# Optimization experiments

Measured on AMD Instinct MI355X. Metric: run time of the kernel, lower is better.

## Reference

```python
import jax, jax.numpy as jnp
import numpy as np

N_NODES = 40000
N_EDGES = 640000
D = 128
BN_EPS = 1e-5


def setup_inputs() -> dict:
    key = jax.random.key(0)
    k1, k2, k3, k4 = jax.random.split(key, 4)
    x = jax.random.normal(k1, (N_NODES, D), dtype=jnp.float32)
    edge_index = jax.random.randint(k2, (2, N_EDGES), 0, N_NODES, dtype=jnp.int64)
    W = jax.random.normal(k3, (D, D), dtype=jnp.float32) * (1.0 / np.sqrt(D))
    b = jax.random.normal(k4, (D,), dtype=jnp.float32) * 0.01
    gamma = jnp.ones((D,), dtype=jnp.float32)
    beta = jnp.zeros((D,), dtype=jnp.float32)
    return {"x": x, "edge_index": edge_index, "W": W, "b": b,
            "gamma": gamma, "beta": beta}


def reference(x, edge_index, W, b, gamma, beta):
    num_nodes = x.shape[0]
    # linear projection: [N, D_in] @ [D_in, D_out]
    h = x @ W.T + b
    src, dst = edge_index[0], edge_index[1]
    # gather messages from source nodes, scatter-add into destinations
    msgs = jax.ops.segment_sum(h[src], dst, num_segments=num_nodes)  # [N, D]
    # in-degree of each destination node, clamped to >= 1
    deg = jax.ops.segment_sum(jnp.ones_like(dst, dtype=h.dtype), dst,
                              num_segments=num_nodes)
    deg = jnp.maximum(deg, 1.0)
    h = h + msgs / deg[:, None]
    # BatchNorm1d (training mode: biased batch statistics over nodes)
    mean = jnp.mean(h, axis=0)
    var = jnp.mean(jnp.square(h - mean), axis=0)
    out = (h - mean) * jax.lax.rsqrt(var + BN_EPS) * gamma + beta
    return jax.nn.relu(out)
```

## Files before the change

### kernel.cpp

```cpp
#include <hip/hip_runtime.h>

#define NN 40000
#define NE 640000
#define DD 128
#define MAXDEG 64
#define BN_EPS 1e-5f

typedef __attribute__((ext_vector_type(8))) short short8;
typedef __attribute__((ext_vector_type(4))) float f32x4;

__device__ __forceinline__ unsigned int rb16(float x) {
  unsigned int u = __float_as_uint(x);
  return (u + 0x7fffu + ((u >> 16) & 1u)) >> 16;
}

#define PADK 136
__global__ __launch_bounds__(256) void gemm_kernel(
    const float* __restrict__ x, const float* __restrict__ W,
    const float* __restrict__ bias, unsigned int* __restrict__ hbf) {
  __shared__ unsigned short xs[128 * PADK];
  __shared__ unsigned short ws[128 * PADK];
  const int tid = threadIdx.x;
  const int node0 = blockIdx.x * 128;

#pragma unroll
  for (int it = 0; it < 16; ++it) {
    const int flat = it * 256 + tid;
    const int row = flat >> 5;
    const int c4 = flat & 31;
    const int gn = node0 + row;
    float4 v = make_float4(0.f, 0.f, 0.f, 0.f);
    if (gn < NN) v = *reinterpret_cast<const float4*>(x + (size_t)gn * DD + c4 * 4);
    ushort4 p;
    p.x = (unsigned short)rb16(v.x);
    p.y = (unsigned short)rb16(v.y);
    p.z = (unsigned short)rb16(v.z);
    p.w = (unsigned short)rb16(v.w);
    *reinterpret_cast<ushort4*>(&xs[row * PADK + c4 * 4]) = p;
    const float4 wv = *reinterpret_cast<const float4*>(W + (size_t)row * DD + c4 * 4);
    ushort4 q;
    q.x = (unsigned short)rb16(wv.x);
    q.y = (unsigned short)rb16(wv.y);
    q.z = (unsigned short)rb16(wv.z);
    q.w = (unsigned short)rb16(wv.w);
    *reinterpret_cast<ushort4*>(&ws[row * PADK + c4 * 4]) = q;
  }
  __syncthreads();

  const int wave = tid >> 6;
  const int lane = tid & 63;
  const int m = lane & 15;
  const int g = lane >> 4;
  f32x4 acc[2][8];
#pragma unroll
  for (int t = 0; t < 2; ++t)
#pragma unroll
    for (int ct = 0; ct < 8; ++ct) acc[t][ct] = (f32x4){0.f, 0.f, 0.f, 0.f};

#pragma unroll
  for (int ks = 0; ks < 4; ++ks) {
    const int ko = ks * 32 + g * 8;
    short8 a[2], b[8];
#pragma unroll
    for (int t = 0; t < 2; ++t)
      a[t] = *reinterpret_cast<const short8*>(&xs[(wave * 32 + t * 16 + m) * PADK + ko]);
#pragma unroll
    for (int ct = 0; ct < 8; ++ct)
      b[ct] = *reinterpret_cast<const short8*>(&ws[(ct * 16 + m) * PADK + ko]);
#pragma unroll
    for (int t = 0; t < 2; ++t)
#pragma unroll
      for (int ct = 0; ct < 8; ++ct)
        acc[t][ct] = __builtin_amdgcn_mfma_f32_16x16x32_bf16(a[t], b[ct], acc[t][ct], 0, 0, 0);
  }
  __syncthreads();

#pragma unroll
  for (int t = 0; t < 2; ++t) {
#pragma unroll
    for (int ct = 0; ct < 8; ++ct) {
      const int ch = ct * 16 + m;
      const float bv = bias[ch];
#pragma unroll
      for (int reg = 0; reg < 4; ++reg) {
        const int nrow = wave * 32 + t * 16 + g * 4 + reg;
        xs[nrow * PADK + ch] = (unsigned short)rb16(acc[t][ct][reg] + bv);
      }
    }
  }
  __syncthreads();
#pragma unroll
  for (int it = 0; it < 8; ++it) {
    const int flat = it * 256 + tid;
    const int row = flat >> 4;
    const int c8 = flat & 15;
    const int gn = node0 + row;
    if (gn < NN) {
      const uint4 o = *reinterpret_cast<const uint4*>(&xs[row * PADK + c8 * 8]);
      *reinterpret_cast<uint4*>(hbf + (size_t)gn * 64 + c8 * 4) = o;
    }
  }
}

__global__ __launch_bounds__(256) void bucket_kernel(
    const int* __restrict__ ei, int* __restrict__ cursors,
    unsigned short* __restrict__ esorted) {
  const int e = blockIdx.x * 256 + threadIdx.x;
  if (e < NE) {
    const int s = ei[e];
    const int d = ei[NE + e];
    const int p = atomicAdd(&cursors[d], 1);
    if (p < MAXDEG) esorted[(size_t)d * MAXDEG + p] = (unsigned short)s;
  }
}

__global__ __launch_bounds__(256) void gather_kernel(
    const unsigned int* __restrict__ hbf,
    const unsigned short* __restrict__ esorted, const int* __restrict__ cursors,
    float* __restrict__ v_out, float* __restrict__ sums) {
  const int tid = threadIdx.x;
  const int wv = tid >> 6;
  const int lane = tid & 63;
  const int q = lane >> 4;
  const int c = lane & 15;
  const int nWaves = gridDim.x * 4;
  float s8[8], q8[8];
#pragma unroll
  for (int j = 0; j < 8; ++j) { s8[j] = 0.f; q8[j] = 0.f; }

  for (int n = blockIdx.x * 4 + wv; n < NN; n += nWaves) {
    const int deg = cursors[n];
    const int dcl = min(deg, MAXDEG);
    const int base = n * MAXDEG;
    float acc[8];
#pragma unroll
    for (int j = 0; j < 8; ++j) acc[j] = 0.f;

    for (int i0 = 0; i0 < dcl; i0 += 16) {
      int id[4];
      float w[4];
#pragma unroll
      for (int j = 0; j < 4; ++j) {
        const int e = i0 + q + 4 * j;
        const int raw = (int)esorted[base + min(e, MAXDEG - 1)];
        const bool vld = e < dcl;
        id[j] = vld ? raw : n;
        w[j] = vld ? 1.f : 0.f;
      }
#pragma unroll
      for (int j = 0; j < 4; ++j) {
        const uint4 u = *reinterpret_cast<const uint4*>(hbf + (size_t)id[j] * 64 + c * 4);
        acc[0] = fmaf(__uint_as_float(u.x << 16), w[j], acc[0]);
        acc[1] = fmaf(__uint_as_float(u.x & 0xffff0000u), w[j], acc[1]);
        acc[2] = fmaf(__uint_as_float(u.y << 16), w[j], acc[2]);
        acc[3] = fmaf(__uint_as_float(u.y & 0xffff0000u), w[j], acc[3]);
        acc[4] = fmaf(__uint_as_float(u.z << 16), w[j], acc[4]);
        acc[5] = fmaf(__uint_as_float(u.z & 0xffff0000u), w[j], acc[5]);
        acc[6] = fmaf(__uint_as_float(u.w << 16), w[j], acc[6]);
        acc[7] = fmaf(__uint_as_float(u.w & 0xffff0000u), w[j], acc[7]);
      }
    }
#pragma unroll
    for (int j = 0; j < 8; ++j) {
      acc[j] += __shfl_xor(acc[j], 16, 64);
      acc[j] += __shfl_xor(acc[j], 32, 64);
    }
    if (q == 0) {
      const float rdeg = 1.0f / (float)max(deg, 1);
      const uint4 su = *reinterpret_cast<const uint4*>(hbf + (size_t)n * 64 + c * 4);
      float v[8];
      v[0] = __uint_as_float(su.x << 16) + acc[0] * rdeg;
      v[1] = __uint_as_float(su.x & 0xffff0000u) + acc[1] * rdeg;
      v[2] = __uint_as_float(su.y << 16) + acc[2] * rdeg;
      v[3] = __uint_as_float(su.y & 0xffff0000u) + acc[3] * rdeg;
      v[4] = __uint_as_float(su.z << 16) + acc[4] * rdeg;
      v[5] = __uint_as_float(su.z & 0xffff0000u) + acc[5] * rdeg;
      v[6] = __uint_as_float(su.w << 16) + acc[6] * rdeg;
      v[7] = __uint_as_float(su.w & 0xffff0000u) + acc[7] * rdeg;
      *reinterpret_cast<float4*>(v_out + (size_t)n * DD + c * 8) =
          make_float4(v[0], v[1], v[2], v[3]);
      *reinterpret_cast<float4*>(v_out + (size_t)n * DD + c * 8 + 4) =
          make_float4(v[4], v[5], v[6], v[7]);
#pragma unroll
      for (int j = 0; j < 8; ++j) {
        s8[j] += v[j];
        q8[j] += v[j] * v[j];
      }
    }
  }
  __shared__ float redS[4][128];
  __shared__ float redQ[4][128];
  if (q == 0) {
#pragma unroll
    for (int j = 0; j < 8; ++j) {
      redS[wv][c * 8 + j] = s8[j];
      redQ[wv][c * 8 + j] = q8[j];
    }
  }
  __syncthreads();
  if (tid < 128) {
    const float S = redS[0][tid] + redS[1][tid] + redS[2][tid] + redS[3][tid];
    const float Q = redQ[0][tid] + redQ[1][tid] + redQ[2][tid] + redQ[3][tid];
    const int r = blockIdx.x & 7;
    unsafeAtomicAdd(&sums[r * 256 + tid], S);
    unsafeAtomicAdd(&sums[r * 256 + 128 + tid], Q);
  }
}

__global__ __launch_bounds__(256) void normalize_kernel(
    const float* __restrict__ sums, const float* __restrict__ gamma,
    const float* __restrict__ beta, float* __restrict__ out) {
  __shared__ float sc[128];
  __shared__ float sh[128];
  const int tid = threadIdx.x;
  if (tid < 128) {
    float S = 0.f, Q = 0.f;
#pragma unroll
    for (int r = 0; r < 8; ++r) {
      S += sums[r * 256 + tid];
      Q += sums[r * 256 + 128 + tid];
    }
    const float inv_n = 1.0f / (float)NN;
    const float mean = S * inv_n;
    const float var = Q * inv_n - mean * mean;
    const float inv = rsqrtf(var + BN_EPS);
    const float g = gamma[tid] * inv;
    sc[tid] = g;
    sh[tid] = beta[tid] - mean * g;
  }
  __syncthreads();
  const long total4 = (long)NN * DD / 4;
  for (long i = blockIdx.x * 256L + tid; i < total4; i += (long)gridDim.x * 256L) {
    const int c4 = (int)(i & 31);
    const float4 v = *reinterpret_cast<const float4*>(out + i * 4);
    const float4 scv = *reinterpret_cast<const float4*>(&sc[c4 * 4]);
    const float4 shv = *reinterpret_cast<const float4*>(&sh[c4 * 4]);
    float4 o;
    o.x = fmaxf(v.x * scv.x + shv.x, 0.f);
    o.y = fmaxf(v.y * scv.y + shv.y, 0.f);
    o.z = fmaxf(v.z * scv.z + shv.z, 0.f);
    o.w = fmaxf(v.w * scv.w + shv.w, 0.f);
    *reinterpret_cast<float4*>(out + i * 4) = o;
  }
}

extern "C" void kernel_launch(void* const* d_in, const int* in_sizes, int n_in,
                              void* d_out, int out_size, void* d_ws, size_t ws_size,
                              hipStream_t stream) {
  const float* x     = (const float*)d_in[0];
  const int*   ei    = (const int*)d_in[1];
  const float* W     = (const float*)d_in[2];
  const float* b     = (const float*)d_in[3];
  const float* gamma = (const float*)d_in[4];
  const float* beta  = (const float*)d_in[5];
  float* out = (float*)d_out;

  unsigned int*   hbf     = (unsigned int*)d_ws;
  unsigned short* esorted = (unsigned short*)(hbf + (size_t)NN * 64);
  int*            cursors = (int*)(esorted + (size_t)NN * MAXDEG);
  float*          sums    = (float*)(cursors + NN);

  hipMemsetAsync(cursors, 0, (size_t)(NN + 8 * 256) * sizeof(int), stream);

  gemm_kernel<<<(NN + 127) / 128, 256, 0, stream>>>(x, W, b, hbf);
  bucket_kernel<<<(NE + 255) / 256, 256, 0, stream>>>(ei, cursors, esorted);
  gather_kernel<<<2560, 256, 0, stream>>>(hbf, esorted, cursors, out, sums);
  normalize_kernel<<<1280, 256, 0, stream>>>(sums, gamma, beta, out);
}
```

Before: 156.6 us.

## Fuse bucketing, gather and batchnorm into one cooperative grid-synced kernel

Replaces the memset, bucket, gather and normalize launches with a single cooperative kernel that zeroes the counters, buckets edges, gathers neighbours, reduces statistics and normalizes, separated by grid.sync barriers. Each wave loads its node's neighbour list once into registers and broadcasts indices by shuffle, and prefetches the next node's degree and list while working on the current one. This removes launch gaps and repeated per-iteration esorted loads. In exchange, the grid is limited to occupancy-sized persistent blocks (capped at 1024), and grid-wide barriers add cost. A fallback runs the old multi-kernel path if the cooperative launch fails.

```diff
diff --git a/kernel.cpp b/kernel.cpp
--- a/kernel.cpp
+++ b/kernel.cpp
@@ -1,10 +1,14 @@
 #include <hip/hip_runtime.h>
+#include <hip/hip_cooperative_groups.h>
+
+namespace cg = cooperative_groups;
 
 #define NN 40000
 #define NE 640000
 #define DD 128
 #define MAXDEG 64
 #define BN_EPS 1e-5f
+#define MAXBLK 1024
 
 typedef __attribute__((ext_vector_type(8))) short short8;
 typedef __attribute__((ext_vector_type(4))) float f32x4;
@@ -102,6 +106,168 @@
   }
 }
 
+__device__ __forceinline__ void gather_node(
+    const unsigned int* __restrict__ hbf, int n, int deg, int sraw,
+    int q, int c, float* __restrict__ vout8, bool* wrote) {
+  const int dcl = min(deg, MAXDEG);
+  float acc[8];
+#pragma unroll
+  for (int j = 0; j < 8; ++j) acc[j] = 0.f;
+  for (int i0 = 0; i0 < dcl; i0 += 16) {
+    int id[4];
+    float w[4];
+#pragma unroll
+    for (int j = 0; j < 4; ++j) {
+      const int e = i0 + q + 4 * j;
+      const int idv = __shfl(sraw, min(e, MAXDEG - 1), 64);
+      const bool vld = e < dcl;
+      id[j] = vld ? idv : n;
+      w[j] = vld ? 1.f : 0.f;
+    }
+#pragma unroll
+    for (int j = 0; j < 4; ++j) {
+      const uint4 u = *reinterpret_cast<const uint4*>(hbf + (size_t)id[j] * 64 + c * 4);
+      acc[0] = fmaf(__uint_as_float(u.x << 16), w[j], acc[0]);
+      acc[1] = fmaf(__uint_as_float(u.x & 0xffff0000u), w[j], acc[1]);
+      acc[2] = fmaf(__uint_as_float(u.y << 16), w[j], acc[2]);
+      acc[3] = fmaf(__uint_as_float(u.y & 0xffff0000u), w[j], acc[3]);
+      acc[4] = fmaf(__uint_as_float(u.z << 16), w[j], acc[4]);
+      acc[5] = fmaf(__uint_as_float(u.z & 0xffff0000u), w[j], acc[5]);
+      acc[6] = fmaf(__uint_as_float(u.w << 16), w[j], acc[6]);
+      acc[7] = fmaf(__uint_as_float(u.w & 0xffff0000u), w[j], acc[7]);
+    }
+  }
+#pragma unroll
+  for (int j = 0; j < 8; ++j) {
+    acc[j] += __shfl_xor(acc[j], 16, 64);
+    acc[j] += __shfl_xor(acc[j], 32, 64);
+  }
+  *wrote = (q == 0);
+  if (q == 0) {
+    const float rdeg = 1.0f / (float)max(deg, 1);
+    const uint4 su = *reinterpret_cast<const uint4*>(hbf + (size_t)n * 64 + c * 4);
+    vout8[0] = __uint_as_float(su.x << 16) + acc[0] * rdeg;
+    vout8[1] = __uint_as_float(su.x & 0xffff0000u) + acc[1] * rdeg;
+    vout8[2] = __uint_as_float(su.y << 16) + acc[2] * rdeg;
+    vout8[3] = __uint_as_float(su.y & 0xffff0000u) + acc[3] * rdeg;
+    vout8[4] = __uint_as_float(su.z << 16) + acc[4] * rdeg;
+    vout8[5] = __uint_as_float(su.z & 0xffff0000u) + acc[5] * rdeg;
+    vout8[6] = __uint_as_float(su.w << 16) + acc[6] * rdeg;
+    vout8[7] = __uint_as_float(su.w & 0xffff0000u) + acc[7] * rdeg;
+  }
+}
+
+__global__ __launch_bounds__(256, 4) void fused_kernel(
+    const int* __restrict__ ei, const unsigned int* __restrict__ hbf,
+    unsigned short* __restrict__ esorted, int* __restrict__ cursors,
+    float* __restrict__ sums, const float* __restrict__ gamma,
+    const float* __restrict__ beta, float* __restrict__ out) {
+  cg::grid_group grid = cg::this_grid();
+  const int tid = threadIdx.x;
+  const int bid = blockIdx.x;
+  const int gsz = gridDim.x * 256;
+  const int gt = bid * 256 + tid;
+
+  for (int i = gt; i < NN + 8 * 256; i += gsz) cursors[i] = 0;
+  grid.sync();
+
+  for (int e = gt; e < NE; e += gsz) {
+    const int s = ei[e];
+    const int d = ei[NE + e];
+    const int p = atomicAdd(&cursors[d], 1);
+    if (p < MAXDEG) esorted[d * MAXDEG + p] = (unsigned short)s;
+  }
+  grid.sync();
+
+  const int wv = tid >> 6;
+  const int lane = tid & 63;
+  const int q = lane >> 4;
+  const int c = lane & 15;
+  const int nW = gridDim.x * 4;
+  const int wid = bid * 4 + wv;
+  float s8[8], q8[8];
+#pragma unroll
+  for (int j = 0; j < 8; ++j) { s8[j] = 0.f; q8[j] = 0.f; }
+
+  int n = wid;
+  int deg = 0, sraw = 0;
+  if (n < NN) {
+    deg = cursors[n];
+    sraw = (int)esorted[n * MAXDEG + lane];
+  }
+  while (n < NN) {
+    const int n2 = n + nW;
+    int deg2 = 0, sraw2 = 0;
+    if (n2 < NN) {
+      deg2 = cursors[n2];
+      sraw2 = (int)esorted[n2 * MAXDEG + lane];
+    }
+    float v[8];
+    bool wrote;
+    gather_node(hbf, n, deg, sraw, q, c, v, &wrote);
+    if (wrote) {
+      *reinterpret_cast<float4*>(out + (size_t)n * DD + c * 8) =
+          make_float4(v[0], v[1], v[2], v[3]);
+      *reinterpret_cast<float4*>(out + (size_t)n * DD + c * 8 + 4) =
+          make_float4(v[4], v[5], v[6], v[7]);
+#pragma unroll
+      for (int j = 0; j < 8; ++j) {
+        s8[j] += v[j];
+        q8[j] += v[j] * v[j];
+      }
+    }
+    n = n2;
+    deg = deg2;
+    sraw = sraw2;
+  }
+  __shared__ float redS[4][128];
+  __shared__ float redQ[4][128];
+  if (q == 0) {
+#pragma unroll
+    for (int j = 0; j < 8; ++j) {
+      redS[wv][c * 8 + j] = s8[j];
+      redQ[wv][c * 8 + j] = q8[j];
+    }
+  }
+  __syncthreads();
+  if (tid < 128) {
+    const float S = redS[0][tid] + redS[1][tid] + redS[2][tid] + redS[3][tid];
+    const float Q = redQ[0][tid] + redQ[1][tid] + redQ[2][tid] + redQ[3][tid];
+    const int r = bid & 7;
+    unsafeAtomicAdd(&sums[r * 256 + tid], S);
+    unsafeAtomicAdd(&sums[r * 256 + 128 + tid], Q);
+  }
+  grid.sync();
+
+  __shared__ float sc[128];
+  __shared__ float sh[128];
+  if (tid < 128) {
+    float S = 0.f, Q = 0.f;
+#pragma unroll
+    for (int r = 0; r < 8; ++r) {
+      S += sums[r * 256 + tid];
+      Q += sums[r * 256 + 128 + tid];
+    }
+    const float inv_n = 1.0f / (float)NN;
+    const float mean = S * inv_n;
+    const float var = Q * inv_n - mean * mean;
+    const float inv = rsqrtf(var + BN_EPS);
+    const float g = gamma[tid] * inv;
+    sc[tid] = g;
+    sh[tid] = beta[tid] - mean * g;
+  }
+  __syncthreads();
+  const int ch = lane * 2;
+  const float2 scv = make_float2(sc[ch], sc[ch + 1]);
+  const float2 shv = make_float2(sh[ch], sh[ch + 1]);
+  for (int nn = wid; nn < NN; nn += nW) {
+    float2 v = *reinterpret_cast<const float2*>(out + (size_t)nn * DD + ch);
+    v.x = fmaxf(v.x * scv.x + shv.x, 0.f);
+    v.y = fmaxf(v.y * scv.y + shv.y, 0.f);
+    *reinterpret_cast<float2*>(out + (size_t)nn * DD + ch) = v;
+  }
+}
+
 __global__ __launch_bounds__(256) void bucket_kernel(
     const int* __restrict__ ei, int* __restrict__ cursors,
     unsigned short* __restrict__ esorted) {
@@ -110,7 +276,7 @@
     const int s = ei[e];
     const int d = ei[NE + e];
     const int p = atomicAdd(&cursors[d], 1);
-    if (p < MAXDEG) esorted[(size_t)d * MAXDEG + p] = (unsigned short)s;
+    if (p < MAXDEG) esorted[d * MAXDEG + p] = (unsigned short)s;
   }
 }
 
@@ -123,60 +289,18 @@
   const int lane = tid & 63;
   const int q = lane >> 4;
   const int c = lane & 15;
-  const int nWaves = gridDim.x * 4;
+  const int nW = gridDim.x * 4;
+  const int wid = blockIdx.x * 4 + wv;
   float s8[8], q8[8];
 #pragma unroll
   for (int j = 0; j < 8; ++j) { s8[j] = 0.f; q8[j] = 0.f; }
-
-  for (int n = blockIdx.x * 4 + wv; n < NN; n += nWaves) {
+  for (int n = wid; n < NN; n += nW) {
     const int deg = cursors[n];
-    const int dcl = min(deg, MAXDEG);
-    const int base = n * MAXDEG;
-    float acc[8];
-#pragma unroll
-    for (int j = 0; j < 8; ++j) acc[j] = 0.f;
-
-    for (int i0 = 0; i0 < dcl; i0 += 16) {
-      int id[4];
-      float w[4];
-#pragma unroll
-      for (int j = 0; j < 4; ++j) {
-        const int e = i0 + q + 4 * j;
-        const int raw = (int)esorted[base + min(e, MAXDEG - 1)];
-        const bool vld = e < dcl;
-        id[j] = vld ? raw : n;
-        w[j] = vld ? 1.f : 0.f;
-      }
-#pragma unroll
-      for (int j = 0; j < 4; ++j) {
-        const uint4 u = *reinterpret_cast<const uint4*>(hbf + (size_t)id[j] * 64 + c * 4);
-        acc[0] = fmaf(__uint_as_float(u.x << 16), w[j], acc[0]);
-        acc[1] = fmaf(__uint_as_float(u.x & 0xffff0000u), w[j], acc[1]);
-        acc[2] = fmaf(__uint_as_float(u.y << 16), w[j], acc[2]);
-        acc[3] = fmaf(__uint_as_float(u.y & 0xffff0000u), w[j], acc[3]);
-        acc[4] = fmaf(__uint_as_float(u.z << 16), w[j], acc[4]);
-        acc[5] = fmaf(__uint_as_float(u.z & 0xffff0000u), w[j], acc[5]);
-        acc[6] = fmaf(__uint_as_float(u.w << 16), w[j], acc[6]);
-        acc[7] = fmaf(__uint_as_float(u.w & 0xffff0000u), w[j], acc[7]);
-      }
-    }
-#pragma unroll
-    for (int j = 0; j < 8; ++j) {
-      acc[j] += __shfl_xor(acc[j], 16, 64);
-      acc[j] += __shfl_xor(acc[j], 32, 64);
-    }
-    if (q == 0) {
-      const float rdeg = 1.0f / (float)max(deg, 1);
-      const uint4 su = *reinterpret_cast<const uint4*>(hbf + (size_t)n * 64 + c * 4);
-      float v[8];
-      v[0] = __uint_as_float(su.x << 16) + acc[0] * rdeg;
-      v[1] = __uint_as_float(su.x & 0xffff0000u) + acc[1] * rdeg;
-      v[2] = __uint_as_float(su.y << 16) + acc[2] * rdeg;
-      v[3] = __uint_as_float(su.y & 0xffff0000u) + acc[3] * rdeg;
-      v[4] = __uint_as_float(su.z << 16) + acc[4] * rdeg;
-      v[5] = __uint_as_float(su.z & 0xffff0000u) + acc[5] * rdeg;
-      v[6] = __uint_as_float(su.w << 16) + acc[6] * rdeg;
-      v[7] = __uint_as_float(su.w & 0xffff0000u) + acc[7] * rdeg;
+    const int sraw = (int)esorted[n * MAXDEG + lane];
+    float v[8];
+    bool wrote;
+    gather_node(hbf, n, deg, sraw, q, c, v, &wrote);
+    if (wrote) {
       *reinterpret_cast<float4*>(v_out + (size_t)n * DD + c * 8) =
           make_float4(v[0], v[1], v[2], v[3]);
       *reinterpret_cast<float4*>(v_out + (size_t)n * DD + c * 8 + 4) =
@@ -260,10 +384,25 @@
   int*            cursors = (int*)(esorted + (size_t)NN * MAXDEG);
   float*          sums    = (float*)(cursors + NN);
 
-  hipMemsetAsync(cursors, 0, (size_t)(NN + 8 * 256) * sizeof(int), stream);
-
   gemm_kernel<<<(NN + 127) / 128, 256, 0, stream>>>(x, W, b, hbf);
-  bucket_kernel<<<(NE + 255) / 256, 256, 0, stream>>>(ei, cursors, esorted);
-  gather_kernel<<<2560, 256, 0, stream>>>(hbf, esorted, cursors, out, sums);
-  normalize_kernel<<<1280, 256, 0, stream>>>(sums, gamma, beta, out);
-}
+
+  int occ = 0;
+  hipError_t qerr =
+      hipOccupancyMaxActiveBlocksPerMultiprocessor(&occ, fused_kernel, 256, 0);
+  int nblk = (qerr == hipSuccess && occ > 0) ? occ * 256 : 0;
+  if (nblk > MAXBLK) nblk = MAXBLK;
+
+  hipError_t lerr = hipErrorUnknown;
+  if (nblk > 0) {
+    void* args[] = {(void*)&ei, (void*)&hbf, (void*)&esorted, (void*)&cursors,
+                    (void*)&sums, (void*)&gamma, (void*)&beta, (void*)&out};
+    lerr = hipLaunchCooperativeKernel(fused_kernel, dim3(nblk), dim3(256), args,
+                                      0, stream);
+  }
+  if (lerr != hipSuccess) {
+    hipMemsetAsync(cursors, 0, (size_t)(NN + 8 * 256) * sizeof(int), stream);
+    bucket_kernel<<<(NE + 255) / 256, 256, 0, stream>>>(ei, cursors, esorted);
+    gather_kernel<<<2560, 256, 0, stream>>>(hbf, esorted, cursors, out, sums);
+    normalize_kernel<<<1280, 256, 0, stream>>>(sums, gamma, beta, out);
+  }
+}
```

Measured after the change: 345.7 us. 121% more time.

## Fuse GEMM and edge bucketing into one launch; prefetch next node in gather

Applied to the files above, without the earlier changes.

The GEMM and the edge-bucketing kernels are merged into one launch, with extra blocks doing grid-strided bucketing so the two independent stages can run at the same time and one launch is saved. The gather kernel now loads each node's whole neighbor list with one coalesced per-lane read and hands indices out by wave shuffle instead of repeated scalar loads. It also software-prefetches the next node's degree, neighbor list and self row. The risks are extra register pressure and the bucketing blocks, which use no shared memory, still reserving the GEMM kernel's large shared allocation.

```diff
diff --git a/kernel.cpp b/kernel.cpp
--- a/kernel.cpp
+++ b/kernel.cpp
@@ -5,6 +5,9 @@
 #define DD 128
 #define MAXDEG 64
 #define BN_EPS 1e-5f
+#define GEMM_BLKS 313
+#define BUCKET_BLKS 320
+#define PADK 136
 
 typedef __attribute__((ext_vector_type(8))) short short8;
 typedef __attribute__((ext_vector_type(4))) float f32x4;
@@ -14,15 +17,27 @@
   return (u + 0x7fffu + ((u >> 16) & 1u)) >> 16;
 }
 
-#define PADK 136
-__global__ __launch_bounds__(256) void gemm_kernel(
+__global__ __launch_bounds__(256) void fat_kernel(
     const float* __restrict__ x, const float* __restrict__ W,
-    const float* __restrict__ bias, unsigned int* __restrict__ hbf) {
+    const float* __restrict__ bias, unsigned int* __restrict__ hbf,
+    const int* __restrict__ ei, int* __restrict__ cursors,
+    unsigned short* __restrict__ esorted) {
   __shared__ unsigned short xs[128 * PADK];
   __shared__ unsigned short ws[128 * PADK];
   const int tid = threadIdx.x;
+
+  if (blockIdx.x >= GEMM_BLKS) {
+    const int b = blockIdx.x - GEMM_BLKS;
+    for (int e = b * 256 + tid; e < NE; e += BUCKET_BLKS * 256) {
+      const int s = ei[e];
+      const int d = ei[NE + e];
+      const int p = atomicAdd(&cursors[d], 1);
+      if (p < MAXDEG) esorted[d * MAXDEG + p] = (unsigned short)s;
+    }
+    return;
+  }
+
   const int node0 = blockIdx.x * 128;
-
 #pragma unroll
   for (int it = 0; it < 16; ++it) {
     const int flat = it * 256 + tid;
@@ -102,18 +117,6 @@
   }
 }
 
-__global__ __launch_bounds__(256) void bucket_kernel(
-    const int* __restrict__ ei, int* __restrict__ cursors,
-    unsigned short* __restrict__ esorted) {
-  const int e = blockIdx.x * 256 + threadIdx.x;
-  if (e < NE) {
-    const int s = ei[e];
-    const int d = ei[NE + e];
-    const int p = atomicAdd(&cursors[d], 1);
-    if (p < MAXDEG) esorted[(size_t)d * MAXDEG + p] = (unsigned short)s;
-  }
-}
-
 __global__ __launch_bounds__(256) void gather_kernel(
     const unsigned int* __restrict__ hbf,
     const unsigned short* __restrict__ esorted, const int* __restrict__ cursors,
@@ -123,28 +126,42 @@
   const int lane = tid & 63;
   const int q = lane >> 4;
   const int c = lane & 15;
-  const int nWaves = gridDim.x * 4;
+  const int nW = gridDim.x * 4;
+  const int wid = blockIdx.x * 4 + wv;
   float s8[8], q8[8];
 #pragma unroll
   for (int j = 0; j < 8; ++j) { s8[j] = 0.f; q8[j] = 0.f; }
 
-  for (int n = blockIdx.x * 4 + wv; n < NN; n += nWaves) {
-    const int deg = cursors[n];
+  int n = wid;
+  int deg = 0, sraw = 0;
+  uint4 su = make_uint4(0u, 0u, 0u, 0u);
+  if (n < NN) {
+    deg = cursors[n];
+    sraw = (int)esorted[n * MAXDEG + lane];
+    su = *reinterpret_cast<const uint4*>(hbf + (size_t)n * 64 + c * 4);
+  }
+  while (n < NN) {
+    const int n2 = n + nW;
+    int deg2 = 0, sraw2 = 0;
+    uint4 su2 = make_uint4(0u, 0u, 0u, 0u);
+    if (n2 < NN) {
+      deg2 = cursors[n2];
+      sraw2 = (int)esorted[n2 * MAXDEG + lane];
+      su2 = *reinterpret_cast<const uint4*>(hbf + (size_t)n2 * 64 + c * 4);
+    }
     const int dcl = min(deg, MAXDEG);
-    const int base = n * MAXDEG;
     float acc[8];
 #pragma unroll
     for (int j = 0; j < 8; ++j) acc[j] = 0.f;
-
     for (int i0 = 0; i0 < dcl; i0 += 16) {
       int id[4];
       float w[4];
 #pragma unroll
       for (int j = 0; j < 4; ++j) {
         const int e = i0 + q + 4 * j;
-        const int raw = (int)esorted[base + min(e, MAXDEG - 1)];
+        const int idv = __shfl(sraw, min(e, MAXDEG - 1), 64);
         const bool vld = e < dcl;
-        id[j] = vld ? raw : n;
+        id[j] = vld ? idv : n;
         w[j] = vld ? 1.f : 0.f;
       }
 #pragma unroll
@@ -167,7 +184,6 @@
     }
     if (q == 0) {
       const float rdeg = 1.0f / (float)max(deg, 1);
-      const uint4 su = *reinterpret_cast<const uint4*>(hbf + (size_t)n * 64 + c * 4);
       float v[8];
       v[0] = __uint_as_float(su.x << 16) + acc[0] * rdeg;
       v[1] = __uint_as_float(su.x & 0xffff0000u) + acc[1] * rdeg;
@@ -187,6 +203,10 @@
         q8[j] += v[j] * v[j];
       }
     }
+    n = n2;
+    deg = deg2;
+    sraw = sraw2;
+    su = su2;
   }
   __shared__ float redS[4][128];
   __shared__ float redQ[4][128];
@@ -261,9 +281,8 @@
   float*          sums    = (float*)(cursors + NN);
 
   hipMemsetAsync(cursors, 0, (size_t)(NN + 8 * 256) * sizeof(int), stream);
-
-  gemm_kernel<<<(NN + 127) / 128, 256, 0, stream>>>(x, W, b, hbf);
-  bucket_kernel<<<(NE + 255) / 256, 256, 0, stream>>>(ei, cursors, esorted);
+  fat_kernel<<<GEMM_BLKS + BUCKET_BLKS, 256, 0, stream>>>(x, W, b, hbf, ei,
+                                                          cursors, esorted);
   gather_kernel<<<2560, 256, 0, stream>>>(hbf, esorted, cursors, out, sums);
   normalize_kernel<<<1280, 256, 0, stream>>>(sums, gamma, beta, out);
 }
```

Result: faster. 145.9 us (-6.8%).

## Fuse edge bucketing into gather via per-block shared-memory scans; pre-convert W

Applied to the files above, without the earlier changes.

Drops the global atomic bucket kernel and the cursor memset. Each of 256 blocks scans the full destination array and bins the edges whose destinations fall in its own node range into shared-memory slots, then gathers for those nodes. W is converted to bf16 once by a small prep kernel, which also zeroes the sums, and the GEMM reads W straight from global memory instead of staging it in LDS. The cost is that every block rereads the whole 2.5 MB edge-destination array, which amounts to about 650 MB of mostly-L2 traffic in total. Only 256 blocks of 1024 threads are used, which may leave parallelism and occupancy short.

```diff
diff --git a/kernel.cpp b/kernel.cpp
--- a/kernel.cpp
+++ b/kernel.cpp
@@ -3,8 +3,11 @@
 #define NN 40000
 #define NE 640000
 #define DD 128
-#define MAXDEG 64
 #define BN_EPS 1e-5f
+#define GEMM_BLKS 313
+#define PADK 132
+#define SG_BLOCKS 256
+#define NPB 157
 
 typedef __attribute__((ext_vector_type(8))) short short8;
 typedef __attribute__((ext_vector_type(4))) float f32x4;
@@ -14,15 +17,21 @@
   return (u + 0x7fffu + ((u >> 16) & 1u)) >> 16;
 }
 
-#define PADK 136
+__global__ __launch_bounds__(256) void prep_kernel(
+    const float* __restrict__ W, unsigned short* __restrict__ wbf,
+    float* __restrict__ sums) {
+  const int gt = blockIdx.x * 256 + threadIdx.x;
+  const int gsz = gridDim.x * 256;
+  for (int i = gt; i < 8 * 256; i += gsz) sums[i] = 0.f;
+  for (int i = gt; i < DD * DD; i += gsz) wbf[i] = (unsigned short)rb16(W[i]);
+}
+
 __global__ __launch_bounds__(256) void gemm_kernel(
-    const float* __restrict__ x, const float* __restrict__ W,
+    const float* __restrict__ x, const unsigned short* __restrict__ wbf,
     const float* __restrict__ bias, unsigned int* __restrict__ hbf) {
   __shared__ unsigned short xs[128 * PADK];
-  __shared__ unsigned short ws[128 * PADK];
   const int tid = threadIdx.x;
   const int node0 = blockIdx.x * 128;
-
 #pragma unroll
   for (int it = 0; it < 16; ++it) {
     const int flat = it * 256 + tid;
@@ -37,13 +46,6 @@
     p.z = (unsigned short)rb16(v.z);
     p.w = (unsigned short)rb16(v.w);
     *reinterpret_cast<ushort4*>(&xs[row * PADK + c4 * 4]) = p;
-    const float4 wv = *reinterpret_cast<const float4*>(W + (size_t)row * DD + c4 * 4);
-    ushort4 q;
-    q.x = (unsigned short)rb16(wv.x);
-    q.y = (unsigned short)rb16(wv.y);
-    q.z = (unsigned short)rb16(wv.z);
-    q.w = (unsigned short)rb16(wv.w);
-    *reinterpret_cast<ushort4*>(&ws[row * PADK + c4 * 4]) = q;
   }
   __syncthreads();
 
@@ -66,7 +68,7 @@
       a[t] = *reinterpret_cast<const short8*>(&xs[(wave * 32 + t * 16 + m) * PADK + ko]);
 #pragma unroll
     for (int ct = 0; ct < 8; ++ct)
-      b[ct] = *reinterpret_cast<const short8*>(&ws[(ct * 16 + m) * PADK + ko]);
+      b[ct] = *reinterpret_cast<const short8*>(wbf + (ct * 16 + m) * DD + ko);
 #pragma unroll
     for (int t = 0; t < 2; ++t)
 #pragma unroll
@@ -102,49 +104,64 @@
   }
 }
 
-__global__ __launch_bounds__(256) void bucket_kernel(
-    const int* __restrict__ ei, int* __restrict__ cursors,
-    unsigned short* __restrict__ esorted) {
-  const int e = blockIdx.x * 256 + threadIdx.x;
-  if (e < NE) {
-    const int s = ei[e];
-    const int d = ei[NE + e];
-    const int p = atomicAdd(&cursors[d], 1);
-    if (p < MAXDEG) esorted[(size_t)d * MAXDEG + p] = (unsigned short)s;
-  }
-}
-
-__global__ __launch_bounds__(256) void gather_kernel(
-    const unsigned int* __restrict__ hbf,
-    const unsigned short* __restrict__ esorted, const int* __restrict__ cursors,
-    float* __restrict__ v_out, float* __restrict__ sums) {
+__global__ __launch_bounds__(1024) void scangather_kernel(
+    const int* __restrict__ ei, const unsigned int* __restrict__ hbf,
+    float* __restrict__ out, float* __restrict__ sums) {
+  __shared__ unsigned short slots[NPB * 64];
+  __shared__ int cnt[NPB];
+  __shared__ float redS[16][128];
+  __shared__ float redQ[16][128];
   const int tid = threadIdx.x;
+  const int lo = blockIdx.x * NPB;
+  const int hi = min(lo + NPB, NN);
+  const int nloc = hi - lo;
+
+  for (int i = tid; i < NPB; i += 1024) cnt[i] = 0;
+  __syncthreads();
+
+  const int4* d4 = reinterpret_cast<const int4*>(ei + NE);
+  const int* srcA = ei;
+  const int nch = NE / 4;
+  for (int idx = tid; idx < nch; idx += 1024) {
+    const int4 dv = d4[idx];
+    const int e = idx * 4;
+#pragma unroll
+    for (int j = 0; j < 4; ++j) {
+      const int d = (j == 0) ? dv.x : (j == 1) ? dv.y : (j == 2) ? dv.z : dv.w;
+      const int dl = d - lo;
+      if (dl >= 0 && dl < nloc) {
+        const int p = atomicAdd(&cnt[dl], 1);
+        if (p < 64) slots[dl * 64 + p] = (unsigned short)srcA[e + j];
+      }
+    }
+  }
+  __syncthreads();
+
   const int wv = tid >> 6;
   const int lane = tid & 63;
   const int q = lane >> 4;
   const int c = lane & 15;
-  const int nWaves = gridDim.x * 4;
   float s8[8], q8[8];
 #pragma unroll
   for (int j = 0; j < 8; ++j) { s8[j] = 0.f; q8[j] = 0.f; }
 
-  for (int n = blockIdx.x * 4 + wv; n < NN; n += nWaves) {
-    const int deg = cursors[n];
-    const int dcl = min(deg, MAXDEG);
-    const int base = n * MAXDEG;
+  for (int nl = wv; nl < nloc; nl += 16) {
+    const int n = lo + nl;
+    const int deg = cnt[nl];
+    const int dcl = min(deg, 64);
+    const uint4 su = *reinterpret_cast<const uint4*>(hbf + (size_t)n * 64 + c * 4);
     float acc[8];
 #pragma unroll
     for (int j = 0; j < 8; ++j) acc[j] = 0.f;
-
     for (int i0 = 0; i0 < dcl; i0 += 16) {
       int id[4];
       float w[4];
 #pragma unroll
       for (int j = 0; j < 4; ++j) {
         const int e = i0 + q + 4 * j;
-        const int raw = (int)esorted[base + min(e, MAXDEG - 1)];
+        const int sv = (int)slots[nl * 64 + min(e, 63)];
         const bool vld = e < dcl;
-        id[j] = vld ? raw : n;
+        id[j] = vld ? sv : n;
         w[j] = vld ? 1.f : 0.f;
       }
 #pragma unroll
@@ -167,7 +184,6 @@
     }
     if (q == 0) {
       const float rdeg = 1.0f / (float)max(deg, 1);
-      const uint4 su = *reinterpret_cast<const uint4*>(hbf + (size_t)n * 64 + c * 4);
       float v[8];
       v[0] = __uint_as_float(su.x << 16) + acc[0] * rdeg;
       v[1] = __uint_as_float(su.x & 0xffff0000u) + acc[1] * rdeg;
@@ -177,9 +193,9 @@
       v[5] = __uint_as_float(su.z & 0xffff0000u) + acc[5] * rdeg;
       v[6] = __uint_as_float(su.w << 16) + acc[6] * rdeg;
       v[7] = __uint_as_float(su.w & 0xffff0000u) + acc[7] * rdeg;
-      *reinterpret_cast<float4*>(v_out + (size_t)n * DD + c * 8) =
+      *reinterpret_cast<float4*>(out + (size_t)n * DD + c * 8) =
           make_float4(v[0], v[1], v[2], v[3]);
-      *reinterpret_cast<float4*>(v_out + (size_t)n * DD + c * 8 + 4) =
+      *reinterpret_cast<float4*>(out + (size_t)n * DD + c * 8 + 4) =
           make_float4(v[4], v[5], v[6], v[7]);
 #pragma unroll
       for (int j = 0; j < 8; ++j) {
@@ -188,8 +204,6 @@
       }
     }
   }
-  __shared__ float redS[4][128];
-  __shared__ float redQ[4][128];
   if (q == 0) {
 #pragma unroll
     for (int j = 0; j < 8; ++j) {
@@ -199,8 +213,9 @@
   }
   __syncthreads();
   if (tid < 128) {
-    const float S = redS[0][tid] + redS[1][tid] + redS[2][tid] + redS[3][tid];
-    const float Q = redQ[0][tid] + redQ[1][tid] + redQ[2][tid] + redQ[3][tid];
+    float S = 0.f, Q = 0.f;
+#pragma unroll
+    for (int i = 0; i < 16; ++i) { S += redS[i][tid]; Q += redQ[i][tid]; }
     const int r = blockIdx.x & 7;
     unsafeAtomicAdd(&sums[r * 256 + tid], S);
     unsafeAtomicAdd(&sums[r * 256 + 128 + tid], Q);
@@ -255,15 +270,12 @@
   const float* beta  = (const float*)d_in[5];
   float* out = (float*)d_out;
 
-  unsigned int*   hbf     = (unsigned int*)d_ws;
-  unsigned short* esorted = (unsigned short*)(hbf + (size_t)NN * 64);
-  int*            cursors = (int*)(esorted + (size_t)NN * MAXDEG);
-  float*          sums    = (float*)(cursors + NN);
-
-  hipMemsetAsync(cursors, 0, (size_t)(NN + 8 * 256) * sizeof(int), stream);
-
-  gemm_kernel<<<(NN + 127) / 128, 256, 0, stream>>>(x, W, b, hbf);
-  bucket_kernel<<<(NE + 255) / 256, 256, 0, stream>>>(ei, cursors, esorted);
-  gather_kernel<<<2560, 256, 0, stream>>>(hbf, esorted, cursors, out, sums);
+  unsigned int*   hbf = (unsigned int*)d_ws;
+  float*          sums = (float*)(hbf + (size_t)NN * 64);
+  unsigned short* wbf = (unsigned short*)(sums + 8 * 256);
+
+  prep_kernel<<<64, 256, 0, stream>>>(W, wbf, sums);
+  gemm_kernel<<<GEMM_BLKS, 256, 0, stream>>>(x, wbf, b, hbf);
+  scangather_kernel<<<SG_BLOCKS, 1024, 0, stream>>>(ei, hbf, out, sums);
   normalize_kernel<<<1280, 256, 0, stream>>>(sums, gamma, beta, out);
 }
```

Result: slower. 213.9 us (+36.6%).
